# Kernel tuning notes

Hardware: AMD Instinct MI355X
Metric: run time of the kernel (lower is better)

## Reference

```python
import jax, jax.numpy as jnp
import numpy as np

N, L, H, DH = 4, 1024, 16, 64
D = H * DH  # 1024
DFF = 4 * D
NEG_INF = jnp.float32(-1e30)  # used via actual -inf per torch masked_fill


def layer_norm(x, g, b, eps=1e-5):
    mu = jnp.mean(x, axis=-1, keepdims=True)
    var = jnp.mean(jnp.square(x - mu), axis=-1, keepdims=True)
    return (x - mu) * jax.lax.rsqrt(var + eps) * g + b


def mha(q_in, k_in, Wq, Wk, Wv, mask, padding_mask):
    # q_in: (N,Lq,D), k_in: (N,Lk,D); Linear weights (D,D), out = x @ W.T
    n, Lq, _ = q_in.shape
    Lk = k_in.shape[1]
    q = jnp.einsum('nld,od->nlo', q_in, Wq).reshape(n, Lq, H, DH)
    k = jnp.einsum('nld,od->nlo', k_in, Wk).reshape(n, Lk, H, DH)
    v = jnp.einsum('nld,od->nlo', k_in, Wv).reshape(n, Lk, H, DH)
    # per-sample scaling = sqrt(#non-padded keys)
    scaling = jnp.sqrt(jnp.sum(~padding_mask, axis=-1).astype(q.dtype))  # (N,)
    score = jnp.einsum('nqhd,nkhd->nhqk', q, k) / scaling[:, None, None, None]
    if mask is not None:
        score = jnp.where(mask[None, None, :, :], -jnp.inf, score)
    score = jnp.where(padding_mask[:, None, None, :], -jnp.inf, score)
    p = jax.nn.softmax(score, axis=-1)
    out = jnp.einsum('nhqk,nkhd->nqhd', p, v).reshape(n, Lq, D)
    return out


def setup_inputs() -> dict:
    key = jax.random.key(0)
    ks = jax.random.split(key, 16)
    s = 0.02
    inp = {
        'encoded': jax.random.normal(ks[0], (N, L, D), jnp.float32),
        'Y': jax.random.normal(ks[1], (N, L, D), jnp.float32),
        # causal mask: True above diagonal -> attention set to -inf
        'mask': ~jnp.tril(jnp.ones((L, L), dtype=bool)),
        # suffix padding with varied per-sample lengths (all >= 1)
        'padding_mask': jnp.arange(L)[None, :] >= jnp.array([L, 3 * L // 4, L // 2, 7 * L // 8])[:, None],
        # masked self-attention projections
        'Wq1': jax.random.normal(ks[2], (D, D), jnp.float32) * s,
        'Wk1': jax.random.normal(ks[3], (D, D), jnp.float32) * s,
        'Wv1': jax.random.normal(ks[4], (D, D), jnp.float32) * s,
        'g1': jnp.ones((D,), jnp.float32), 'b1': jnp.zeros((D,), jnp.float32),
        # cross-attention projections
        'Wq2': jax.random.normal(ks[5], (D, D), jnp.float32) * s,
        'Wk2': jax.random.normal(ks[6], (D, D), jnp.float32) * s,
        'Wv2': jax.random.normal(ks[7], (D, D), jnp.float32) * s,
        'g2': jnp.ones((D,), jnp.float32), 'b2': jnp.zeros((D,), jnp.float32),
        # FFN
        'We': jax.random.normal(ks[8], (DFF, D), jnp.float32) * s,
        'be': jnp.zeros((DFF,), jnp.float32),
        'Wc': jax.random.normal(ks[9], (D, DFF), jnp.float32) * s,
        'bc': jnp.zeros((D,), jnp.float32),
        'g3': jnp.ones((D,), jnp.float32), 'b3': jnp.zeros((D,), jnp.float32),
    }
    return inp


def reference(encoded, Y, mask, padding_mask,
              Wq1, Wk1, Wv1, g1, b1,
              Wq2, Wk2, Wv2, g2, b2,
              We, be, Wc, bc, g3, b3):
    # masked self-attention + residual + LN (dropout=0 -> identity)
    res = Y
    a = mha(Y, Y, Wq1, Wk1, Wv1, mask, padding_mask)
    Y = layer_norm(a + res, g1, b1)
    # cross-attention (no causal mask) + residual + LN
    res = Y
    a = mha(Y, encoded, Wq2, Wk2, Wv2, None, padding_mask)
    Y = layer_norm(a + res, g2, b2)
    # FFN + residual + LN
    res = Y
    h = jax.nn.relu(jnp.einsum('nld,fd->nlf', Y, We) + be)
    h = jnp.einsum('nlf,df->nld', h, Wc) + bc
    Y = layer_norm(h + res, g3, b3)
    return Y
```

## Files before the change

kernel.cpp:

```cpp
#include <hip/hip_runtime.h>
#include <stdint.h>

#define NB 4
#define LS 1024
#define HH 16
#define DHD 64
#define DM 1024
#define DF 4096
#define QKS 2048
#define LOG2E 1.4426950408889634f

typedef unsigned short u16;
typedef __attribute__((ext_vector_type(4))) float f32x4;
typedef __attribute__((ext_vector_type(8))) __bf16 bf16x8;
typedef __attribute__((ext_vector_type(8))) unsigned short u16x8;

__device__ __forceinline__ u16 f2bf(float f) {
  union { float f; uint32_t u; } v; v.f = f;
  uint32_t u = v.u;
  return (u16)((u + 0x7fffu + ((u >> 16) & 1u)) >> 16);
}

__device__ __forceinline__ bf16x8 ldb8(const u16* p) {
  u16x8 r = *(const u16x8*)p;
  return __builtin_bit_cast(bf16x8, r);
}

__device__ __forceinline__ void gload_lds16(const u16* g, u16* l) {
  __builtin_amdgcn_global_load_lds((const __attribute__((address_space(1))) void*)g,
                                   (__attribute__((address_space(3))) void*)l,
                                   16, 0, 0);
}

#define WAITV8() asm volatile("s_waitcnt vmcnt(8)" ::: "memory")
#define WAITV0() asm volatile("s_waitcnt vmcnt(0)" ::: "memory")
#define WAITLGKM() asm volatile("s_waitcnt lgkmcnt(0)" ::: "memory")
#define PHASE_BARRIER()                        \
  do {                                         \
    WAITLGKM();                                \
    __builtin_amdgcn_sched_barrier(0);         \
    __builtin_amdgcn_s_barrier();              \
    __builtin_amdgcn_sched_barrier(0);         \
  } while (0)

__global__ void prep_kernel(const uint32_t* __restrict__ pm, int* lens, float* iscl) {
  __shared__ int flagByte;
  __shared__ int red[256];
  const int tid = threadIdx.x, n = blockIdx.x;
  if (tid == 0) flagByte = 0;
  __syncthreads();
  int f = 0;
  for (int w = tid; w < (NB * LS) / 4; w += 256) {
    uint32_t u = pm[w];
    if (u != 0u && u != 1u && u != 0x3f800000u) f = 1;
  }
  if (f) atomicOr(&flagByte, 1);
  __syncthreads();
  int c = 0;
  if (flagByte) {
    const uint8_t* pb = (const uint8_t*)pm;
    for (int l = tid; l < LS; l += 256) c += (pb[n * LS + l] == 0) ? 1 : 0;
  } else {
    for (int l = tid; l < LS; l += 256) c += (pm[n * LS + l] == 0) ? 1 : 0;
  }
  red[tid] = c;
  __syncthreads();
  for (int s = 128; s > 0; s >>= 1) {
    if (tid < s) red[tid] += red[tid + s];
    __syncthreads();
  }
  if (tid == 0) { lens[n] = red[0]; iscl[n] = 1.0f / sqrtf((float)red[0]); }
}

__global__ void cvt_all(const float* s0, u16* d0, const float* s1, u16* d1,
                        const float* s2, u16* d2, const float* s3, u16* d3,
                        const float* s4, u16* d4, const float* s5, u16* d5,
                        const float* s6, u16* d6, const float* s7, u16* d7,
                        const float* s8, u16* d8, const float* s9, u16* d9) {
  const int total = 5767168;
  int i = blockIdx.x * 256 + threadIdx.x;
  for (; i < total; i += gridDim.x * 256) {
    const float* s; u16* d; int j;
    if (i < 1048576)      { s = s0; d = d0; j = i; }
    else if (i < 2097152) { s = s1; d = d1; j = i - 1048576; }
    else if (i < 2359296) { s = s2; d = d2; j = i - 2097152; }
    else if (i < 2621440) { s = s3; d = d3; j = i - 2359296; }
    else if (i < 2883584) { s = s4; d = d4; j = i - 2621440; }
    else if (i < 3145728) { s = s5; d = d5; j = i - 2883584; }
    else if (i < 3407872) { s = s6; d = d6; j = i - 3145728; }
    else if (i < 3670016) { s = s7; d = d7; j = i - 3407872; }
    else if (i < 4718592) { s = s8; d = d8; j = i - 3670016; }
    else                  { s = s9; d = d9; j = i - 4718592; }
    float4 fv = ((const float4*)s)[j];
    ushort4 o;
    o.x = f2bf(fv.x); o.y = f2bf(fv.y); o.z = f2bf(fv.z); o.w = f2bf(fv.w);
    ((ushort4*)d)[j] = o;
  }
}

template <int MODE>
__global__ __launch_bounds__(512, 2) void gemm8(
    const u16* __restrict__ P0, const u16* __restrict__ P1,
    const u16* __restrict__ PW, const float* __restrict__ bias,
    void* __restrict__ O0, void* __restrict__ O1,
    void* __restrict__ O2, void* __restrict__ O3,
    const float* __restrict__ iscl) {
  extern __shared__ u16 lds[];
  constexpr int NT = 16;
  const int bm = blockIdx.x;
  const int tid = threadIdx.x;
  const int wid = tid >> 6, lane = tid & 63;
  const int lrow = lane & 15, lgrp = lane >> 4;
  const int wm = wid >> 2, wn = wid & 3;

  const u16* Asrc; const u16* Bsrc; int lda, ldb;
  if constexpr (MODE == 0) {
    Asrc = P0 + (size_t)bm * 256 * DM; lda = DM;
    Bsrc = PW + (size_t)blockIdx.y * 256 * DM; ldb = DM;
  } else if constexpr (MODE == 1) {
    const int z = blockIdx.z;
    Asrc = P0 + (size_t)bm * 256 * DF + z * 1024; lda = DF;
    Bsrc = PW + (size_t)blockIdx.y * 256 * DF + z * 1024; ldb = DF;
  } else {
    const int bnt = blockIdx.y;
    Asrc = (bnt < 12 ? P0 : P1) + (size_t)bm * 256 * DM; lda = DM;
    const int wrow = (bnt < 12) ? bnt * 256 : 4096 + (bnt - 12) * 256;
    Bsrc = PW + (size_t)wrow * DM; ldb = DM;
  }

  int srow[2], skk[2];
#pragma unroll
  for (int i = 0; i < 2; i++) {
    const int c = (i * 8 + wid) * 64 + lane;
    const int pair = c >> 3;
    const int ue = ((c & 7) * 8) ^ ((pair & 7) << 3);
    srow[i] = pair * 2 + (ue >> 5);
    skk[i] = ue & 31;
  }
  const int dslot0 = wid * 512;
  const int dslot1 = (8 + wid) * 512;

  f32x4 acc[2][4][4] = {};

  auto STAGE_A = [&](int kt, int buf, int kh) {
    const int ks = kt < NT ? kt : NT - 1;
    gload_lds16(Asrc + (size_t)srow[0] * lda + ks * 64 + kh * 32 + skk[0],
                lds + buf * 16384 + kh * 8192 + dslot0);
    gload_lds16(Asrc + (size_t)srow[1] * lda + ks * 64 + kh * 32 + skk[1],
                lds + buf * 16384 + kh * 8192 + dslot1);
  };
  auto STAGE_B = [&](int kt, int buf, int kh) {
    const int ks = kt < NT ? kt : NT - 1;
    gload_lds16(Bsrc + (size_t)srow[0] * ldb + ks * 64 + kh * 32 + skk[0],
                lds + 32768 + buf * 16384 + kh * 8192 + dslot0);
    gload_lds16(Bsrc + (size_t)srow[1] * ldb + ks * 64 + kh * 32 + skk[1],
                lds + 32768 + buf * 16384 + kh * 8192 + dslot1);
  };
  auto LDA = [&](int buf, int kh, int mh, bf16x8* a) {
#pragma unroll
    for (int m = 0; m < 4; m++) {
      const int row = wm * 128 + mh * 64 + m * 16 + lrow;
      const int idx = buf * 16384 + kh * 8192 + (row >> 1) * 64 +
                      ((((row & 1) << 5) + (lgrp << 3)) ^ (((row >> 1) & 7) << 3));
      a[m] = ldb8(lds + idx);
    }
  };
  auto LDB = [&](int buf, int kh, bf16x8* b) {
#pragma unroll
    for (int nn = 0; nn < 4; nn++) {
      const int row = wn * 64 + nn * 16 + lrow;
      const int idx = 32768 + buf * 16384 + kh * 8192 + (row >> 1) * 64 +
                      ((((row & 1) << 5) + (lgrp << 3)) ^ (((row >> 1) & 7) << 3));
      b[nn] = ldb8(lds + idx);
    }
  };
  auto MFMA16 = [&](f32x4 (&a4)[4][4], bf16x8* af, bf16x8* bk) {
    __builtin_amdgcn_s_setprio(1);
#pragma unroll
    for (int m = 0; m < 4; m++)
#pragma unroll
      for (int nn = 0; nn < 4; nn++)
        a4[m][nn] = __builtin_amdgcn_mfma_f32_16x16x32_bf16(af[m], bk[nn], a4[m][nn], 0, 0, 0);
    __builtin_amdgcn_s_setprio(0);
  };

  STAGE_A(0, 0, 0); STAGE_B(0, 0, 0);
  STAGE_A(0, 0, 1); STAGE_B(0, 0, 1);
  STAGE_A(1, 1, 0); STAGE_B(1, 1, 0);
  WAITV8();
  __builtin_amdgcn_s_barrier();
  __builtin_amdgcn_sched_barrier(0);

  for (int t = 0; t < NT; t++) {
    const int b = t & 1;
    bf16x8 af[4], bk[4];
    LDA(b, 0, 0, af); LDB(b, 0, bk);
    STAGE_A(t + 1, b ^ 1, 1);
    PHASE_BARRIER();
    MFMA16(acc[0], af, bk);
    LDA(b, 0, 1, af);
    STAGE_B(t + 1, b ^ 1, 1);
    WAITV8();
    PHASE_BARRIER();
    MFMA16(acc[1], af, bk);
    LDA(b, 1, 0, af); LDB(b, 1, bk);
    STAGE_A(t + 2, b, 0);
    PHASE_BARRIER();
    MFMA16(acc[0], af, bk);
    LDA(b, 1, 1, af);
    STAGE_B(t + 2, b, 0);
    WAITV8();
    PHASE_BARRIER();
    MFMA16(acc[1], af, bk);
  }
  WAITV0();

#pragma unroll
  for (int mh = 0; mh < 2; mh++)
#pragma unroll
    for (int m = 0; m < 4; m++) {
      const int grow0 = bm * 256 + wm * 128 + mh * 64 + m * 16 + lgrp * 4;
#pragma unroll
      for (int nn = 0; nn < 4; nn++) {
        const int col_l = wn * 64 + nn * 16 + lrow;
        f32x4 v = acc[mh][m][nn];
        if constexpr (MODE == 0) {
          const int col = blockIdx.y * 256 + col_l;
          const float bv = bias[col];
#pragma unroll
          for (int r = 0; r < 4; r++) {
            float x = v[r] + bv;
            x = x > 0.0f ? x : 0.0f;
            ((u16*)O0)[(size_t)(grow0 + r) * DF + col] = f2bf(x);
          }
        } else if constexpr (MODE == 1) {
          float* C = (float*)O0 + (size_t)blockIdx.z * ((size_t)NB * LS * DM);
          const int col = blockIdx.y * 256 + col_l;
#pragma unroll
          for (int r = 0; r < 4; r++) C[(size_t)(grow0 + r) * DM + col] = v[r];
        } else {
          const int bnt = blockIdx.y;
          const int nidx = grow0 >> 10, l0 = grow0 & 1023;
          if (bnt < 8) {
            const float qs = (bnt < 4) ? iscl[nidx] * LOG2E : 1.0f;
            const int col = bnt * 256 + col_l;
#pragma unroll
            for (int r = 0; r < 4; r++)
              ((u16*)O0)[(size_t)(grow0 + r) * QKS + col] = f2bf(v[r] * qs);
          } else if (bnt < 12) {
            const int vc = (bnt - 8) * 256 + col_l;
            ushort4 o;
            o.x = f2bf(v[0]); o.y = f2bf(v[1]); o.z = f2bf(v[2]); o.w = f2bf(v[3]);
            *(ushort4*)((u16*)O1 + (((size_t)(nidx * HH + (vc >> 6)) * DHD + (vc & 63)) << 10) + l0) = o;
          } else {
            const int col = 1024 + (bnt - 12) * 256 + col_l;
#pragma unroll
            for (int r = 0; r < 4; r++)
              ((u16*)O2)[(size_t)(grow0 + r) * QKS + col] = f2bf(v[r]);
          }
        }
      }
    }
}

__global__ __launch_bounds__(256) void gemm_qv(const u16* __restrict__ Ya,
                                               const u16* __restrict__ Ea,
                                               const u16* __restrict__ Wq,
                                               const u16* __restrict__ Wv,
                                               u16* __restrict__ QKb,
                                               u16* __restrict__ VtB,
                                               const float* __restrict__ iscl) {
  __shared__ u16 Al[128 * 32];
  __shared__ u16 Bl[128 * 32];
  const int tid = threadIdx.x;
  const int bm = blockIdx.x, bnr = blockIdx.y;
  const bool isV = bnr >= 8;
  const int bn = isV ? bnr - 8 : bnr;
  const int wave = tid >> 6, lane = tid & 63;
  const int lrow = lane & 15, lgrp = lane >> 4;
  const int wr = (wave >> 1) * 64, wc = (wave & 1) * 64;
  f32x4 acc[4][4] = {};
  const u16* Ab = (isV ? Ea : Ya) + (size_t)bm * 128 * DM;
  const u16* Bb = (isV ? Wv : Wq) + (size_t)bn * 128 * DM;
  {
    const int c0 = wave, c1 = wave + 4;
    const int r0 = c0 * 16 + (lane >> 2), r1 = c1 * 16 + (lane >> 2);
    const int scc = (lane & 3) * 8;
    const u16* Ag0 = Ab + (size_t)r0 * DM + scc;
    const u16* Ag1 = Ab + (size_t)r1 * DM + scc;
    const u16* Bg0 = Bb + (size_t)r0 * DM + scc;
    const u16* Bg1 = Bb + (size_t)r1 * DM + scc;
    u16* Ad0 = Al + c0 * 512;
    u16* Ad1 = Al + c1 * 512;
    u16* Bd0 = Bl + c0 * 512;
    u16* Bd1 = Bl + c1 * 512;
    for (int kb = 0; kb < DM; kb += 32) {
      gload_lds16(Ag0, Ad0);
      gload_lds16(Ag1, Ad1);
      gload_lds16(Bg0, Bd0);
      gload_lds16(Bg1, Bd1);
      Ag0 += 32; Ag1 += 32; Bg0 += 32; Bg1 += 32;
      __syncthreads();
      bf16x8 af[4], bfr[4];
#pragma unroll
      for (int m = 0; m < 4; m++) af[m] = ldb8(Al + (wr + m * 16 + lrow) * 32 + lgrp * 8);
#pragma unroll
      for (int nn = 0; nn < 4; nn++) bfr[nn] = ldb8(Bl + (wc + nn * 16 + lrow) * 32 + lgrp * 8);
#pragma unroll
      for (int m = 0; m < 4; m++)
#pragma unroll
        for (int nn = 0; nn < 4; nn++)
          acc[m][nn] = __builtin_amdgcn_mfma_f32_16x16x32_bf16(af[m], bfr[nn], acc[m][nn], 0, 0, 0);
      __syncthreads();
    }
  }
#pragma unroll
  for (int m = 0; m < 4; m++) {
    const int row0 = bm * 128 + wr + m * 16 + lgrp * 4;
    const int nidx = row0 >> 10, l0 = row0 & (LS - 1);
#pragma unroll
    for (int nn = 0; nn < 4; nn++) {
      const int col = bn * 128 + wc + nn * 16 + lrow;
      if (!isV) {
        const float qs = iscl[nidx] * LOG2E;
#pragma unroll
        for (int r = 0; r < 4; r++)
          QKb[(size_t)(row0 + r) * QKS + col] = f2bf(acc[m][nn][r] * qs);
      } else {
        const int hh = col >> 6, dd = col & 63;
        ushort4 o;
        o.x = f2bf(acc[m][nn][0]); o.y = f2bf(acc[m][nn][1]);
        o.z = f2bf(acc[m][nn][2]); o.w = f2bf(acc[m][nn][3]);
        *(ushort4*)(VtB + (((size_t)(nidx * HH + hh) * DHD + dd) << 10) + l0) = o;
      }
    }
  }
}

template <bool CAUSAL>
__global__ __launch_bounds__(256) void attn_kernel(const u16* __restrict__ QK,
                                                   const u16* __restrict__ Vt,
                                                   float* __restrict__ Out,
                                                   const int* __restrict__ lens) {
  __shared__ u16 Kl[64 * 72];
  __shared__ u16 Vl[64 * 72];
  __shared__ u16 Pl[4][16 * 72];
  const int n = blockIdx.z, h = blockIdx.y, qb = blockIdx.x * 64;
  const int tid = threadIdx.x, wave = tid >> 6, lane = tid & 63;
  const int lrow = lane & 15, lgrp = lane >> 4;
  const int len = lens[n];
  const int qrow = qb + wave * 16 + lrow;
  const u16* qptr = QK + ((size_t)(n * LS + qrow)) * QKS + h * DHD + lgrp * 8;
  bf16x8 qf0 = ldb8(qptr);
  bf16x8 qf1 = ldb8(qptr + 32);
  f32x4 oacc[4] = {};
  float m_run = -1e30f, l_run = 0.0f;
  const int kend = CAUSAL ? (len < qb + 64 ? len : qb + 64) : len;
  const int srow = tid >> 3, sc = (tid & 7) * 8;
  const u16* kg_base = QK + 1024 + ((size_t)(n * LS)) * QKS + h * DHD + sc;
  const u16* vg_base = Vt + ((size_t)((n * HH + h) * DHD) + srow) * LS + sc;
  u16* pw = Pl[wave];
  u16x8 kreg[2], vreg[2];
  auto LOADKV = [&](int kb) {
#pragma unroll
    for (int i = 0; i < 2; i++) {
      kreg[i] = *(const u16x8*)(kg_base + (size_t)(kb + srow + i * 32) * QKS);
      vreg[i] = *(const u16x8*)(vg_base + (size_t)(i * 32) * LS + kb);
    }
  };
  LOADKV(0);
  for (int kb = 0; kb < kend; kb += 64) {
    __syncthreads();
#pragma unroll
    for (int i = 0; i < 2; i++) {
      *(u16x8*)(Kl + (srow + i * 32) * 72 + sc) = kreg[i];
      *(u16x8*)(Vl + (srow + i * 32) * 72 + sc) = vreg[i];
    }
    __syncthreads();
    if (kb + 64 < kend) LOADKV(kb + 64);
    f32x4 s[4];
#pragma unroll
    for (int st = 0; st < 4; st++) {
      const u16* kr = Kl + (st * 16 + lrow) * 72 + lgrp * 8;
      bf16x8 kf0 = ldb8(kr);
      bf16x8 kf1 = ldb8(kr + 32);
      f32x4 z = {};
      z = __builtin_amdgcn_mfma_f32_16x16x32_bf16(kf0, qf0, z, 0, 0, 0);
      s[st] = __builtin_amdgcn_mfma_f32_16x16x32_bf16(kf1, qf1, z, 0, 0, 0);
    }
    const bool needMask = (kb + 64 > len) || (CAUSAL && (kb + 64 > qb + wave * 16));
    if (needMask) {
#pragma unroll
      for (int st = 0; st < 4; st++)
#pragma unroll
        for (int r = 0; r < 4; r++) {
          const int k = kb + st * 16 + lgrp * 4 + r;
          bool ok = (k < len) && (!CAUSAL || k <= qrow);
          s[st][r] = ok ? s[st][r] : -1e30f;
        }
    }
    float pmax = s[0][0];
#pragma unroll
    for (int st = 0; st < 4; st++)
#pragma unroll
      for (int r = 0; r < 4; r++) pmax = fmaxf(pmax, s[st][r]);
    pmax = fmaxf(pmax, __shfl_xor(pmax, 16));
    pmax = fmaxf(pmax, __shfl_xor(pmax, 32));
    const bool skip = __all(pmax <= m_run + 11.541560327f);
    float fac = 1.0f;
    if (!skip) {
      float mn = fmaxf(m_run, pmax);
      fac = exp2f(m_run - mn);
      m_run = mn;
    }
    float sm = 0.0f;
#pragma unroll
    for (int st = 0; st < 4; st++)
#pragma unroll
      for (int r = 0; r < 4; r++) {
        float p = exp2f(s[st][r] - m_run);
        s[st][r] = p;
        sm += p;
      }
    sm += __shfl_xor(sm, 16);
    sm += __shfl_xor(sm, 32);
    l_run = l_run * fac + sm;
    if (!skip) {
#pragma unroll
      for (int r = 0; r < 4; r++) {
        float fr = __shfl(fac, (lane & 48) | (lgrp * 4 + r));
#pragma unroll
        for (int dt = 0; dt < 4; dt++) oacc[dt][r] *= fr;
      }
    }
#pragma unroll
    for (int st = 0; st < 4; st++) {
      uint32_t w0, w1;
      asm("v_cvt_pk_bf16_f32 %0, %1, %2" : "=v"(w0) : "v"(s[st][0]), "v"(s[st][1]));
      asm("v_cvt_pk_bf16_f32 %0, %1, %2" : "=v"(w1) : "v"(s[st][2]), "v"(s[st][3]));
      uint2 wv; wv.x = w0; wv.y = w1;
      *(uint2*)(pw + lrow * 72 + st * 16 + lgrp * 4) = wv;
    }
#pragma unroll
    for (int ks = 0; ks < 2; ks++) {
      bf16x8 pf = ldb8(pw + lrow * 72 + ks * 32 + lgrp * 8);
#pragma unroll
      for (int dt = 0; dt < 4; dt++) {
        bf16x8 vf = ldb8(Vl + (dt * 16 + lrow) * 72 + ks * 32 + lgrp * 8);
        oacc[dt] = __builtin_amdgcn_mfma_f32_16x16x32_bf16(pf, vf, oacc[dt], 0, 0, 0);
      }
    }
  }
#pragma unroll
  for (int r = 0; r < 4; r++) {
    float lr = __shfl(l_run, (lane & 48) | (lgrp * 4 + r));
    float inv = 1.0f / lr;
    const int row = qb + wave * 16 + lgrp * 4 + r;
    float* op = Out + ((size_t)(n * LS + row)) * DM + h * DHD;
#pragma unroll
    for (int dt = 0; dt < 4; dt++) op[dt * 16 + lrow] = oacc[dt][r] * inv;
  }
}

__global__ __launch_bounds__(256) void ln_kernel(const float* __restrict__ a,
                                                 const float* __restrict__ res,
                                                 const float* __restrict__ g,
                                                 const float* __restrict__ bta,
                                                 float* __restrict__ outf,
                                                 u16* __restrict__ outb) {
  const int row = blockIdx.x, tid = threadIdx.x;
  float4 x = ((const float4*)(a + (size_t)row * DM))[tid];
  float4 rr = ((const float4*)(res + (size_t)row * DM))[tid];
  x.x += rr.x; x.y += rr.y; x.z += rr.z; x.w += rr.w;
  float s = x.x + x.y + x.z + x.w;
  float s2 = x.x * x.x + x.y * x.y + x.z * x.z + x.w * x.w;
#pragma unroll
  for (int m = 1; m < 64; m <<= 1) { s += __shfl_xor(s, m); s2 += __shfl_xor(s2, m); }
  __shared__ float sm[8];
  const int wv = tid >> 6;
  if ((tid & 63) == 0) { sm[wv] = s; sm[4 + wv] = s2; }
  __syncthreads();
  s = sm[0] + sm[1] + sm[2] + sm[3];
  s2 = sm[4] + sm[5] + sm[6] + sm[7];
  const float mean = s * (1.0f / (float)DM);
  const float var = s2 * (1.0f / (float)DM) - mean * mean;
  const float inv = rsqrtf(var + 1e-5f);
  float4 gg = ((const float4*)g)[tid];
  float4 bb = ((const float4*)bta)[tid];
  float4 y;
  y.x = (x.x - mean) * inv * gg.x + bb.x;
  y.y = (x.y - mean) * inv * gg.y + bb.y;
  y.z = (x.z - mean) * inv * gg.z + bb.z;
  y.w = (x.w - mean) * inv * gg.w + bb.w;
  ((float4*)(outf + (size_t)row * DM))[tid] = y;
  if (outb) {
    ushort4 o;
    o.x = f2bf(y.x); o.y = f2bf(y.y); o.z = f2bf(y.z); o.w = f2bf(y.w);
    ((ushort4*)(outb + (size_t)row * DM))[tid] = o;
  }
}

__global__ __launch_bounds__(256) void ln_final(const float* __restrict__ part,
                                                const float* __restrict__ bias,
                                                const float* __restrict__ res,
                                                const float* __restrict__ g,
                                                const float* __restrict__ bta,
                                                float* __restrict__ outf) {
  const int row = blockIdx.x, tid = threadIdx.x;
  const size_t PS = (size_t)NB * LS * DM;
  float4 x = ((const float4*)(part + (size_t)row * DM))[tid];
  float4 p1 = ((const float4*)(part + PS + (size_t)row * DM))[tid];
  float4 p2 = ((const float4*)(part + 2 * PS + (size_t)row * DM))[tid];
  float4 p3 = ((const float4*)(part + 3 * PS + (size_t)row * DM))[tid];
  float4 bb4 = ((const float4*)bias)[tid];
  float4 rr = ((const float4*)(res + (size_t)row * DM))[tid];
  x.x += p1.x + p2.x + p3.x + bb4.x + rr.x;
  x.y += p1.y + p2.y + p3.y + bb4.y + rr.y;
  x.z += p1.z + p2.z + p3.z + bb4.z + rr.z;
  x.w += p1.w + p2.w + p3.w + bb4.w + rr.w;
  float s = x.x + x.y + x.z + x.w;
  float s2 = x.x * x.x + x.y * x.y + x.z * x.z + x.w * x.w;
#pragma unroll
  for (int m = 1; m < 64; m <<= 1) { s += __shfl_xor(s, m); s2 += __shfl_xor(s2, m); }
  __shared__ float sm[8];
  const int wv = tid >> 6;
  if ((tid & 63) == 0) { sm[wv] = s; sm[4 + wv] = s2; }
  __syncthreads();
  s = sm[0] + sm[1] + sm[2] + sm[3];
  s2 = sm[4] + sm[5] + sm[6] + sm[7];
  const float mean = s * (1.0f / (float)DM);
  const float var = s2 * (1.0f / (float)DM) - mean * mean;
  const float inv = rsqrtf(var + 1e-5f);
  float4 gg = ((const float4*)g)[tid];
  float4 bb = ((const float4*)bta)[tid];
  float4 y;
  y.x = (x.x - mean) * inv * gg.x + bb.x;
  y.y = (x.y - mean) * inv * gg.y + bb.y;
  y.z = (x.z - mean) * inv * gg.z + bb.z;
  y.w = (x.w - mean) * inv * gg.w + bb.w;
  ((float4*)(outf + (size_t)row * DM))[tid] = y;
}

extern "C" void kernel_launch(void* const* d_in, const int* in_sizes, int n_in,
                              void* d_out, int out_size, void* d_ws, size_t ws_size,
                              hipStream_t stream) {
  const float* enc = (const float*)d_in[0];
  const float* Yin = (const float*)d_in[1];
  const uint32_t* pmask = (const uint32_t*)d_in[3];
  const float* Wq1 = (const float*)d_in[4];
  const float* Wk1 = (const float*)d_in[5];
  const float* Wv1 = (const float*)d_in[6];
  const float* g1 = (const float*)d_in[7];
  const float* b1 = (const float*)d_in[8];
  const float* Wq2 = (const float*)d_in[9];
  const float* Wk2 = (const float*)d_in[10];
  const float* Wv2 = (const float*)d_in[11];
  const float* g2 = (const float*)d_in[12];
  const float* b2 = (const float*)d_in[13];
  const float* We = (const float*)d_in[14];
  const float* be = (const float*)d_in[15];
  const float* Wc = (const float*)d_in[16];
  const float* bc = (const float*)d_in[17];
  const float* g3 = (const float*)d_in[18];
  const float* b3 = (const float*)d_in[19];

  const size_t ACT = (size_t)NB * LS * DM;
  const size_t WSZ = (size_t)DM * DM;
  const size_t WFF = (size_t)DF * DM;
  const size_t HID = (size_t)NB * LS * DF;

  char* ws = (char*)d_ws;
  size_t off = 0;
  auto alloc = [&](size_t bytes) -> void* {
    void* p = ws + off;
    off += (bytes + 255) & ~(size_t)255;
    return p;
  };
  int* lens = (int*)alloc(64);
  float* iscl = (float*)alloc(64);
  u16* Ybf = (u16*)alloc(ACT * 2);
  u16* Ebf = (u16*)alloc(ACT * 2);
  u16* W6 = (u16*)alloc(WSZ * 6 * 2);
  u16* Web = (u16*)alloc(WFF * 2);
  u16* Wcb = (u16*)alloc(WFF * 2);
  size_t region0 = off;
  u16* QKa = (u16*)alloc((size_t)NB * LS * QKS * 2);
  u16* VtA = (u16*)alloc(ACT * 2);
  u16* QKb = (u16*)alloc((size_t)NB * LS * QKS * 2);
  u16* VtB = (u16*)alloc(ACT * 2);
  float* aout = (float*)alloc(ACT * 4);
  float* y2 = (float*)alloc(ACT * 4);
  float* part = (float*)(ws + region0);
  float* y3 = (float*)alloc(ACT * 4);
  u16* Hb = (u16*)alloc(HID * 2);

  prep_kernel<<<NB, 256, 0, stream>>>(pmask, lens, iscl);
  cvt_all<<<2048, 256, 0, stream>>>(Yin, Ybf, enc, Ebf,
                                    Wq1, W6 + 0 * WSZ, Wk1, W6 + 1 * WSZ,
                                    Wv1, W6 + 2 * WSZ, Wq2, W6 + 3 * WSZ,
                                    Wk2, W6 + 4 * WSZ, Wv2, W6 + 5 * WSZ,
                                    We, Web, Wc, Wcb);

  dim3 blk(256);
  gemm8<2><<<dim3(16, 16), 512, 131072, stream>>>(Ybf, Ebf, W6, nullptr,
                                                  QKa, VtA, QKb, VtB, iscl);
  attn_kernel<true><<<dim3(16, 16, 4), blk, 0, stream>>>(QKa, VtA, aout, lens);
  ln_kernel<<<NB * LS, 256, 0, stream>>>(aout, Yin, g1, b1, y2, Ybf);
  gemm_qv<<<dim3(32, 16), blk, 0, stream>>>(Ybf, Ebf, W6 + 3 * WSZ, W6 + 5 * WSZ,
                                            QKb, VtB, iscl);
  attn_kernel<false><<<dim3(16, 16, 4), blk, 0, stream>>>(QKb, VtB, aout, lens);
  ln_kernel<<<NB * LS, 256, 0, stream>>>(aout, y2, g2, b2, y3, Ebf);
  gemm8<0><<<dim3(16, 16), 512, 131072, stream>>>(Ebf, nullptr, Web, be,
                                                  Hb, nullptr, nullptr, nullptr, nullptr);
  gemm8<1><<<dim3(16, 4, 4), 512, 131072, stream>>>(Hb, nullptr, Wcb, nullptr,
                                                    part, nullptr, nullptr, nullptr, nullptr);
  ln_final<<<NB * LS, 256, 0, stream>>>(part, bc, y3, g3, b3, (float*)d_out);
}
```

Baseline: 287.5 us.

## Widen attention key tile to 128 and store FFN split-K partials in bf16

```diff
diff --git a/kernel.cpp b/kernel.cpp
--- a/kernel.cpp
+++ b/kernel.cpp
@@ -19,6 +19,11 @@
   union { float f; uint32_t u; } v; v.f = f;
   uint32_t u = v.u;
   return (u16)((u + 0x7fffu + ((u >> 16) & 1u)) >> 16);
+}
+
+__device__ __forceinline__ float b2f(u16 u) {
+  union { uint32_t u; float f; } v; v.u = (uint32_t)u << 16;
+  return v.f;
 }
 
 __device__ __forceinline__ bf16x8 ldb8(const u16* p) {
@@ -234,10 +239,10 @@
             ((u16*)O0)[(size_t)(grow0 + r) * DF + col] = f2bf(x);
           }
         } else if constexpr (MODE == 1) {
-          float* C = (float*)O0 + (size_t)blockIdx.z * ((size_t)NB * LS * DM);
+          u16* C = (u16*)O0 + (size_t)blockIdx.z * ((size_t)NB * LS * DM);
           const int col = blockIdx.y * 256 + col_l;
 #pragma unroll
-          for (int r = 0; r < 4; r++) C[(size_t)(grow0 + r) * DM + col] = v[r];
+          for (int r = 0; r < 4; r++) C[(size_t)(grow0 + r) * DM + col] = f2bf(v[r]);
         } else {
           const int bnt = blockIdx.y;
           const int nidx = grow0 >> 10, l0 = grow0 & 1023;
@@ -342,9 +347,9 @@
                                                    const u16* __restrict__ Vt,
                                                    float* __restrict__ Out,
                                                    const int* __restrict__ lens) {
-  __shared__ u16 Kl[64 * 72];
-  __shared__ u16 Vl[64 * 72];
-  __shared__ u16 Pl[4][16 * 72];
+  __shared__ u16 Kl[128 * 72];
+  __shared__ u16 Vl[64 * 136];
+  __shared__ u16 Pl[4][16 * 136];
   const int n = blockIdx.z, h = blockIdx.y, qb = blockIdx.x * 64;
   const int tid = threadIdx.x, wave = tid >> 6, lane = tid & 63;
   const int lrow = lane & 15, lgrp = lane >> 4;
@@ -356,31 +361,32 @@
   f32x4 oacc[4] = {};
   float m_run = -1e30f, l_run = 0.0f;
   const int kend = CAUSAL ? (len < qb + 64 ? len : qb + 64) : len;
-  const int srow = tid >> 3, sc = (tid & 7) * 8;
-  const u16* kg_base = QK + 1024 + ((size_t)(n * LS)) * QKS + h * DHD + sc;
-  const u16* vg_base = Vt + ((size_t)((n * HH + h) * DHD) + srow) * LS + sc;
+  const u16* kg_base = QK + 1024 + ((size_t)(n * LS + (tid >> 3))) * QKS + h * DHD + (tid & 7) * 8;
+  const u16* vg_base = Vt + ((size_t)((n * HH + h) * DHD) + (tid >> 4)) * LS + (tid & 15) * 8;
+  const int klw = (tid >> 3) * 72 + (tid & 7) * 8;
+  const int vlw = (tid >> 4) * 136 + (tid & 15) * 8;
   u16* pw = Pl[wave];
-  u16x8 kreg[2], vreg[2];
+  u16x8 kreg[4], vreg[4];
   auto LOADKV = [&](int kb) {
 #pragma unroll
-    for (int i = 0; i < 2; i++) {
-      kreg[i] = *(const u16x8*)(kg_base + (size_t)(kb + srow + i * 32) * QKS);
-      vreg[i] = *(const u16x8*)(vg_base + (size_t)(i * 32) * LS + kb);
+    for (int i = 0; i < 4; i++) {
+      kreg[i] = *(const u16x8*)(kg_base + (size_t)(kb + i * 32) * QKS);
+      vreg[i] = *(const u16x8*)(vg_base + (size_t)(i * 16) * LS + kb);
     }
   };
   LOADKV(0);
-  for (int kb = 0; kb < kend; kb += 64) {
+  for (int kb = 0; kb < kend; kb += 128) {
     __syncthreads();
 #pragma unroll
-    for (int i = 0; i < 2; i++) {
-      *(u16x8*)(Kl + (srow + i * 32) * 72 + sc) = kreg[i];
-      *(u16x8*)(Vl + (srow + i * 32) * 72 + sc) = vreg[i];
+    for (int i = 0; i < 4; i++) {
+      *(u16x8*)(Kl + klw + i * (32 * 72)) = kreg[i];
+      *(u16x8*)(Vl + vlw + i * (16 * 136)) = vreg[i];
     }
     __syncthreads();
-    if (kb + 64 < kend) LOADKV(kb + 64);
-    f32x4 s[4];
-#pragma unroll
-    for (int st = 0; st < 4; st++) {
+    if (kb + 128 < kend) LOADKV(kb + 128);
+    f32x4 s[8];
+#pragma unroll
+    for (int st = 0; st < 8; st++) {
       const u16* kr = Kl + (st * 16 + lrow) * 72 + lgrp * 8;
       bf16x8 kf0 = ldb8(kr);
       bf16x8 kf1 = ldb8(kr + 32);
@@ -388,10 +394,10 @@
       z = __builtin_amdgcn_mfma_f32_16x16x32_bf16(kf0, qf0, z, 0, 0, 0);
       s[st] = __builtin_amdgcn_mfma_f32_16x16x32_bf16(kf1, qf1, z, 0, 0, 0);
     }
-    const bool needMask = (kb + 64 > len) || (CAUSAL && (kb + 64 > qb + wave * 16));
+    const bool needMask = (kb + 128 > len) || (CAUSAL && (kb + 128 > qb + wave * 16));
     if (needMask) {
 #pragma unroll
-      for (int st = 0; st < 4; st++)
+      for (int st = 0; st < 8; st++)
 #pragma unroll
         for (int r = 0; r < 4; r++) {
           const int k = kb + st * 16 + lgrp * 4 + r;
@@ -401,7 +407,7 @@
     }
     float pmax = s[0][0];
 #pragma unroll
-    for (int st = 0; st < 4; st++)
+    for (int st = 0; st < 8; st++)
 #pragma unroll
       for (int r = 0; r < 4; r++) pmax = fmaxf(pmax, s[st][r]);
     pmax = fmaxf(pmax, __shfl_xor(pmax, 16));
@@ -415,7 +421,7 @@
     }
     float sm = 0.0f;
 #pragma unroll
-    for (int st = 0; st < 4; st++)
+    for (int st = 0; st < 8; st++)
 #pragma unroll
       for (int r = 0; r < 4; r++) {
         float p = exp2f(s[st][r] - m_run);
@@ -434,19 +440,19 @@
       }
     }
 #pragma unroll
-    for (int st = 0; st < 4; st++) {
+    for (int st = 0; st < 8; st++) {
       uint32_t w0, w1;
       asm("v_cvt_pk_bf16_f32 %0, %1, %2" : "=v"(w0) : "v"(s[st][0]), "v"(s[st][1]));
       asm("v_cvt_pk_bf16_f32 %0, %1, %2" : "=v"(w1) : "v"(s[st][2]), "v"(s[st][3]));
       uint2 wv; wv.x = w0; wv.y = w1;
-      *(uint2*)(pw + lrow * 72 + st * 16 + lgrp * 4) = wv;
-    }
-#pragma unroll
-    for (int ks = 0; ks < 2; ks++) {
-      bf16x8 pf = ldb8(pw + lrow * 72 + ks * 32 + lgrp * 8);
+      *(uint2*)(pw + lrow * 136 + st * 16 + lgrp * 4) = wv;
+    }
+#pragma unroll
+    for (int ks = 0; ks < 4; ks++) {
+      bf16x8 pf = ldb8(pw + lrow * 136 + ks * 32 + lgrp * 8);
 #pragma unroll
       for (int dt = 0; dt < 4; dt++) {
-        bf16x8 vf = ldb8(Vl + (dt * 16 + lrow) * 72 + ks * 32 + lgrp * 8);
+        bf16x8 vf = ldb8(Vl + (dt * 16 + lrow) * 136 + ks * 32 + lgrp * 8);
         oacc[dt] = __builtin_amdgcn_mfma_f32_16x16x32_bf16(pf, vf, oacc[dt], 0, 0, 0);
       }
     }
@@ -500,7 +506,7 @@
   }
 }
 
-__global__ __launch_bounds__(256) void ln_final(const float* __restrict__ part,
+__global__ __launch_bounds__(256) void ln_final(const u16* __restrict__ part,
                                                 const float* __restrict__ bias,
                                                 const float* __restrict__ res,
                                                 const float* __restrict__ g,
@@ -508,16 +514,17 @@
                                                 float* __restrict__ outf) {
   const int row = blockIdx.x, tid = threadIdx.x;
   const size_t PS = (size_t)NB * LS * DM;
-  float4 x = ((const float4*)(part + (size_t)row * DM))[tid];
-  float4 p1 = ((const float4*)(part + PS + (size_t)row * DM))[tid];
-  float4 p2 = ((const float4*)(part + 2 * PS + (size_t)row * DM))[tid];
-  float4 p3 = ((const float4*)(part + 3 * PS + (size_t)row * DM))[tid];
+  ushort4 q0 = ((const ushort4*)(part + (size_t)row * DM))[tid];
+  ushort4 q1 = ((const ushort4*)(part + PS + (size_t)row * DM))[tid];
+  ushort4 q2 = ((const ushort4*)(part + 2 * PS + (size_t)row * DM))[tid];
+  ushort4 q3 = ((const ushort4*)(part + 3 * PS + (size_t)row * DM))[tid];
   float4 bb4 = ((const float4*)bias)[tid];
   float4 rr = ((const float4*)(res + (size_t)row * DM))[tid];
-  x.x += p1.x + p2.x + p3.x + bb4.x + rr.x;
-  x.y += p1.y + p2.y + p3.y + bb4.y + rr.y;
-  x.z += p1.z + p2.z + p3.z + bb4.z + rr.z;
-  x.w += p1.w + p2.w + p3.w + bb4.w + rr.w;
+  float4 x;
+  x.x = b2f(q0.x) + b2f(q1.x) + b2f(q2.x) + b2f(q3.x) + bb4.x + rr.x;
+  x.y = b2f(q0.y) + b2f(q1.y) + b2f(q2.y) + b2f(q3.y) + bb4.y + rr.y;
+  x.z = b2f(q0.z) + b2f(q1.z) + b2f(q2.z) + b2f(q3.z) + bb4.z + rr.z;
+  x.w = b2f(q0.w) + b2f(q1.w) + b2f(q2.w) + b2f(q3.w) + bb4.w + rr.w;
   float s = x.x + x.y + x.z + x.w;
   float s2 = x.x * x.x + x.y * x.y + x.z * x.z + x.w * x.w;
 #pragma unroll
@@ -590,7 +597,7 @@
   u16* VtB = (u16*)alloc(ACT * 2);
   float* aout = (float*)alloc(ACT * 4);
   float* y2 = (float*)alloc(ACT * 4);
-  float* part = (float*)(ws + region0);
+  u16* part = (u16*)(ws + region0);
   float* y3 = (float*)alloc(ACT * 4);
   u16* Hb = (u16*)alloc(HID * 2);
 
```

Result: no change. 291.0 us (+1.2%).

## Double attention query rows per wave and store split-K partials in bf16

Applied to the files above, without the earlier changes.

```diff
diff --git a/kernel.cpp b/kernel.cpp
--- a/kernel.cpp
+++ b/kernel.cpp
@@ -19,6 +19,11 @@
   union { float f; uint32_t u; } v; v.f = f;
   uint32_t u = v.u;
   return (u16)((u + 0x7fffu + ((u >> 16) & 1u)) >> 16);
+}
+
+__device__ __forceinline__ float b2f(u16 u) {
+  union { uint32_t u; float f; } v; v.u = (uint32_t)u << 16;
+  return v.f;
 }
 
 __device__ __forceinline__ bf16x8 ldb8(const u16* p) {
@@ -234,10 +239,10 @@
             ((u16*)O0)[(size_t)(grow0 + r) * DF + col] = f2bf(x);
           }
         } else if constexpr (MODE == 1) {
-          float* C = (float*)O0 + (size_t)blockIdx.z * ((size_t)NB * LS * DM);
+          u16* C = (u16*)O0 + (size_t)blockIdx.z * ((size_t)NB * LS * DM);
           const int col = blockIdx.y * 256 + col_l;
 #pragma unroll
-          for (int r = 0; r < 4; r++) C[(size_t)(grow0 + r) * DM + col] = v[r];
+          for (int r = 0; r < 4; r++) C[(size_t)(grow0 + r) * DM + col] = f2bf(v[r]);
         } else {
           const int bnt = blockIdx.y;
           const int nidx = grow0 >> 10, l0 = grow0 & 1023;
@@ -344,18 +349,20 @@
                                                    const int* __restrict__ lens) {
   __shared__ u16 Kl[64 * 72];
   __shared__ u16 Vl[64 * 72];
-  __shared__ u16 Pl[4][16 * 72];
-  const int n = blockIdx.z, h = blockIdx.y, qb = blockIdx.x * 64;
+  __shared__ u16 Pl[4][32 * 72];
+  const int n = blockIdx.z, h = blockIdx.y, qb = blockIdx.x * 128;
   const int tid = threadIdx.x, wave = tid >> 6, lane = tid & 63;
   const int lrow = lane & 15, lgrp = lane >> 4;
   const int len = lens[n];
-  const int qrow = qb + wave * 16 + lrow;
-  const u16* qptr = QK + ((size_t)(n * LS + qrow)) * QKS + h * DHD + lgrp * 8;
-  bf16x8 qf0 = ldb8(qptr);
-  bf16x8 qf1 = ldb8(qptr + 32);
-  f32x4 oacc[4] = {};
-  float m_run = -1e30f, l_run = 0.0f;
-  const int kend = CAUSAL ? (len < qb + 64 ? len : qb + 64) : len;
+  const int q0 = qb + wave * 32;
+  const int qrowA = q0 + lrow, qrowB = qrowA + 16;
+  const u16* qpA = QK + ((size_t)(n * LS + qrowA)) * QKS + h * DHD + lgrp * 8;
+  const u16* qpB = qpA + (size_t)16 * QKS;
+  bf16x8 qA0 = ldb8(qpA), qA1 = ldb8(qpA + 32);
+  bf16x8 qB0 = ldb8(qpB), qB1 = ldb8(qpB + 32);
+  f32x4 oA[4] = {}, oB[4] = {};
+  float mA = -1e30f, lA = 0.0f, mB = -1e30f, lB = 0.0f;
+  const int kend = CAUSAL ? (len < qb + 128 ? len : qb + 128) : len;
   const int srow = tid >> 3, sc = (tid & 7) * 8;
   const u16* kg_base = QK + 1024 + ((size_t)(n * LS)) * QKS + h * DHD + sc;
   const u16* vg_base = Vt + ((size_t)((n * HH + h) * DHD) + srow) * LS + sc;
@@ -378,87 +385,139 @@
     }
     __syncthreads();
     if (kb + 64 < kend) LOADKV(kb + 64);
-    f32x4 s[4];
+    f32x4 sA[4], sB[4];
 #pragma unroll
     for (int st = 0; st < 4; st++) {
       const u16* kr = Kl + (st * 16 + lrow) * 72 + lgrp * 8;
       bf16x8 kf0 = ldb8(kr);
       bf16x8 kf1 = ldb8(kr + 32);
       f32x4 z = {};
-      z = __builtin_amdgcn_mfma_f32_16x16x32_bf16(kf0, qf0, z, 0, 0, 0);
-      s[st] = __builtin_amdgcn_mfma_f32_16x16x32_bf16(kf1, qf1, z, 0, 0, 0);
-    }
-    const bool needMask = (kb + 64 > len) || (CAUSAL && (kb + 64 > qb + wave * 16));
-    if (needMask) {
+      z = __builtin_amdgcn_mfma_f32_16x16x32_bf16(kf0, qA0, z, 0, 0, 0);
+      sA[st] = __builtin_amdgcn_mfma_f32_16x16x32_bf16(kf1, qA1, z, 0, 0, 0);
+      f32x4 y = {};
+      y = __builtin_amdgcn_mfma_f32_16x16x32_bf16(kf0, qB0, y, 0, 0, 0);
+      sB[st] = __builtin_amdgcn_mfma_f32_16x16x32_bf16(kf1, qB1, y, 0, 0, 0);
+    }
+    if ((kb + 64 > len) || (CAUSAL && (kb + 64 > q0))) {
 #pragma unroll
       for (int st = 0; st < 4; st++)
 #pragma unroll
         for (int r = 0; r < 4; r++) {
           const int k = kb + st * 16 + lgrp * 4 + r;
-          bool ok = (k < len) && (!CAUSAL || k <= qrow);
-          s[st][r] = ok ? s[st][r] : -1e30f;
+          if (!((k < len) && (!CAUSAL || k <= qrowA))) sA[st][r] = -1e30f;
+          if (!((k < len) && (!CAUSAL || k <= qrowB))) sB[st][r] = -1e30f;
         }
     }
-    float pmax = s[0][0];
-#pragma unroll
-    for (int st = 0; st < 4; st++)
-#pragma unroll
-      for (int r = 0; r < 4; r++) pmax = fmaxf(pmax, s[st][r]);
-    pmax = fmaxf(pmax, __shfl_xor(pmax, 16));
-    pmax = fmaxf(pmax, __shfl_xor(pmax, 32));
-    const bool skip = __all(pmax <= m_run + 11.541560327f);
-    float fac = 1.0f;
-    if (!skip) {
-      float mn = fmaxf(m_run, pmax);
-      fac = exp2f(m_run - mn);
-      m_run = mn;
-    }
-    float sm = 0.0f;
-#pragma unroll
-    for (int st = 0; st < 4; st++)
-#pragma unroll
-      for (int r = 0; r < 4; r++) {
-        float p = exp2f(s[st][r] - m_run);
-        s[st][r] = p;
-        sm += p;
+    {
+      float pmax = sA[0][0];
+#pragma unroll
+      for (int st = 0; st < 4; st++)
+#pragma unroll
+        for (int r = 0; r < 4; r++) pmax = fmaxf(pmax, sA[st][r]);
+      pmax = fmaxf(pmax, __shfl_xor(pmax, 16));
+      pmax = fmaxf(pmax, __shfl_xor(pmax, 32));
+      const bool skip = __all(pmax <= mA + 11.541560327f);
+      float fac = 1.0f;
+      if (!skip) {
+        float mn = fmaxf(mA, pmax);
+        fac = exp2f(mA - mn);
+        mA = mn;
       }
-    sm += __shfl_xor(sm, 16);
-    sm += __shfl_xor(sm, 32);
-    l_run = l_run * fac + sm;
-    if (!skip) {
-#pragma unroll
-      for (int r = 0; r < 4; r++) {
-        float fr = __shfl(fac, (lane & 48) | (lgrp * 4 + r));
-#pragma unroll
-        for (int dt = 0; dt < 4; dt++) oacc[dt][r] *= fr;
+      float sm = 0.0f;
+#pragma unroll
+      for (int st = 0; st < 4; st++)
+#pragma unroll
+        for (int r = 0; r < 4; r++) {
+          float p = exp2f(sA[st][r] - mA);
+          sA[st][r] = p;
+          sm += p;
+        }
+      sm += __shfl_xor(sm, 16);
+      sm += __shfl_xor(sm, 32);
+      lA = lA * fac + sm;
+      if (!skip) {
+#pragma unroll
+        for (int r = 0; r < 4; r++) {
+          float fr = __shfl(fac, (lane & 48) | (lgrp * 4 + r));
+#pragma unroll
+          for (int dt = 0; dt < 4; dt++) oA[dt][r] *= fr;
+        }
       }
     }
+    {
+      float pmax = sB[0][0];
+#pragma unroll
+      for (int st = 0; st < 4; st++)
+#pragma unroll
+        for (int r = 0; r < 4; r++) pmax = fmaxf(pmax, sB[st][r]);
+      pmax = fmaxf(pmax, __shfl_xor(pmax, 16));
+      pmax = fmaxf(pmax, __shfl_xor(pmax, 32));
+      const bool skip = __all(pmax <= mB + 11.541560327f);
+      float fac = 1.0f;
+      if (!skip) {
+        float mn = fmaxf(mB, pmax);
+        fac = exp2f(mB - mn);
+        mB = mn;
+      }
+      float sm = 0.0f;
+#pragma unroll
+      for (int st = 0; st < 4; st++)
+#pragma unroll
+        for (int r = 0; r < 4; r++) {
+          float p = exp2f(sB[st][r] - mB);
+          sB[st][r] = p;
+          sm += p;
+        }
+      sm += __shfl_xor(sm, 16);
+      sm += __shfl_xor(sm, 32);
+      lB = lB * fac + sm;
+      if (!skip) {
+#pragma unroll
+        for (int r = 0; r < 4; r++) {
+          float fr = __shfl(fac, (lane & 48) | (lgrp * 4 + r));
+#pragma unroll
+          for (int dt = 0; dt < 4; dt++) oB[dt][r] *= fr;
+        }
+      }
+    }
 #pragma unroll
     for (int st = 0; st < 4; st++) {
-      uint32_t w0, w1;
-      asm("v_cvt_pk_bf16_f32 %0, %1, %2" : "=v"(w0) : "v"(s[st][0]), "v"(s[st][1]));
-      asm("v_cvt_pk_bf16_f32 %0, %1, %2" : "=v"(w1) : "v"(s[st][2]), "v"(s[st][3]));
+      uint32_t w0, w1, x0, x1;
+      asm("v_cvt_pk_bf16_f32 %0, %1, %2" : "=v"(w0) : "v"(sA[st][0]), "v"(sA[st][1]));
+      asm("v_cvt_pk_bf16_f32 %0, %1, %2" : "=v"(w1) : "v"(sA[st][2]), "v"(sA[st][3]));
+      asm("v_cvt_pk_bf16_f32 %0, %1, %2" : "=v"(x0) : "v"(sB[st][0]), "v"(sB[st][1]));
+      asm("v_cvt_pk_bf16_f32 %0, %1, %2" : "=v"(x1) : "v"(sB[st][2]), "v"(sB[st][3]));
       uint2 wv; wv.x = w0; wv.y = w1;
+      uint2 xv; xv.x = x0; xv.y = x1;
       *(uint2*)(pw + lrow * 72 + st * 16 + lgrp * 4) = wv;
+      *(uint2*)(pw + (16 + lrow) * 72 + st * 16 + lgrp * 4) = xv;
     }
 #pragma unroll
     for (int ks = 0; ks < 2; ks++) {
-      bf16x8 pf = ldb8(pw + lrow * 72 + ks * 32 + lgrp * 8);
+      bf16x8 pfA = ldb8(pw + lrow * 72 + ks * 32 + lgrp * 8);
+      bf16x8 pfB = ldb8(pw + (16 + lrow) * 72 + ks * 32 + lgrp * 8);
 #pragma unroll
       for (int dt = 0; dt < 4; dt++) {
         bf16x8 vf = ldb8(Vl + (dt * 16 + lrow) * 72 + ks * 32 + lgrp * 8);
-        oacc[dt] = __builtin_amdgcn_mfma_f32_16x16x32_bf16(pf, vf, oacc[dt], 0, 0, 0);
+        oA[dt] = __builtin_amdgcn_mfma_f32_16x16x32_bf16(pfA, vf, oA[dt], 0, 0, 0);
+        oB[dt] = __builtin_amdgcn_mfma_f32_16x16x32_bf16(pfB, vf, oB[dt], 0, 0, 0);
       }
     }
   }
 #pragma unroll
   for (int r = 0; r < 4; r++) {
-    float lr = __shfl(l_run, (lane & 48) | (lgrp * 4 + r));
-    float inv = 1.0f / lr;
-    const int row = qb + wave * 16 + lgrp * 4 + r;
-    float* op = Out + ((size_t)(n * LS + row)) * DM + h * DHD;
-#pragma unroll
-    for (int dt = 0; dt < 4; dt++) op[dt * 16 + lrow] = oacc[dt][r] * inv;
+    float lrA = __shfl(lA, (lane & 48) | (lgrp * 4 + r));
+    float lrB = __shfl(lB, (lane & 48) | (lgrp * 4 + r));
+    float invA = 1.0f / lrA;
+    float invB = 1.0f / lrB;
+    const int rowA = q0 + lgrp * 4 + r;
+    float* opA = Out + ((size_t)(n * LS + rowA)) * DM + h * DHD;
+    float* opB = opA + (size_t)16 * DM;
+#pragma unroll
+    for (int dt = 0; dt < 4; dt++) {
+      opA[dt * 16 + lrow] = oA[dt][r] * invA;
+      opB[dt * 16 + lrow] = oB[dt][r] * invB;
+    }
   }
 }
 
@@ -500,7 +559,7 @@
   }
 }
 
-__global__ __launch_bounds__(256) void ln_final(const float* __restrict__ part,
+__global__ __launch_bounds__(256) void ln_final(const u16* __restrict__ part,
                                                 const float* __restrict__ bias,
                                                 const float* __restrict__ res,
                                                 const float* __restrict__ g,
@@ -508,16 +567,17 @@
                                                 float* __restrict__ outf) {
   const int row = blockIdx.x, tid = threadIdx.x;
   const size_t PS = (size_t)NB * LS * DM;
-  float4 x = ((const float4*)(part + (size_t)row * DM))[tid];
-  float4 p1 = ((const float4*)(part + PS + (size_t)row * DM))[tid];
-  float4 p2 = ((const float4*)(part + 2 * PS + (size_t)row * DM))[tid];
-  float4 p3 = ((const float4*)(part + 3 * PS + (size_t)row * DM))[tid];
+  ushort4 q0 = ((const ushort4*)(part + (size_t)row * DM))[tid];
+  ushort4 q1 = ((const ushort4*)(part + PS + (size_t)row * DM))[tid];
+  ushort4 q2 = ((const ushort4*)(part + 2 * PS + (size_t)row * DM))[tid];
+  ushort4 q3 = ((const ushort4*)(part + 3 * PS + (size_t)row * DM))[tid];
   float4 bb4 = ((const float4*)bias)[tid];
   float4 rr = ((const float4*)(res + (size_t)row * DM))[tid];
-  x.x += p1.x + p2.x + p3.x + bb4.x + rr.x;
-  x.y += p1.y + p2.y + p3.y + bb4.y + rr.y;
-  x.z += p1.z + p2.z + p3.z + bb4.z + rr.z;
-  x.w += p1.w + p2.w + p3.w + bb4.w + rr.w;
+  float4 x;
+  x.x = b2f(q0.x) + b2f(q1.x) + b2f(q2.x) + b2f(q3.x) + bb4.x + rr.x;
+  x.y = b2f(q0.y) + b2f(q1.y) + b2f(q2.y) + b2f(q3.y) + bb4.y + rr.y;
+  x.z = b2f(q0.z) + b2f(q1.z) + b2f(q2.z) + b2f(q3.z) + bb4.z + rr.z;
+  x.w = b2f(q0.w) + b2f(q1.w) + b2f(q2.w) + b2f(q3.w) + bb4.w + rr.w;
   float s = x.x + x.y + x.z + x.w;
   float s2 = x.x * x.x + x.y * x.y + x.z * x.z + x.w * x.w;
 #pragma unroll
@@ -590,7 +650,7 @@
   u16* VtB = (u16*)alloc(ACT * 2);
   float* aout = (float*)alloc(ACT * 4);
   float* y2 = (float*)alloc(ACT * 4);
-  float* part = (float*)(ws + region0);
+  u16* part = (u16*)(ws + region0);
   float* y3 = (float*)alloc(ACT * 4);
   u16* Hb = (u16*)alloc(HID * 2);
 
@@ -604,11 +664,11 @@
   dim3 blk(256);
   gemm8<2><<<dim3(16, 16), 512, 131072, stream>>>(Ybf, Ebf, W6, nullptr,
                                                   QKa, VtA, QKb, VtB, iscl);
-  attn_kernel<true><<<dim3(16, 16, 4), blk, 0, stream>>>(QKa, VtA, aout, lens);
+  attn_kernel<true><<<dim3(8, 16, 4), blk, 0, stream>>>(QKa, VtA, aout, lens);
   ln_kernel<<<NB * LS, 256, 0, stream>>>(aout, Yin, g1, b1, y2, Ybf);
   gemm_qv<<<dim3(32, 16), blk, 0, stream>>>(Ybf, Ebf, W6 + 3 * WSZ, W6 + 5 * WSZ,
                                             QKb, VtB, iscl);
-  attn_kernel<false><<<dim3(16, 16, 4), blk, 0, stream>>>(QKb, VtB, aout, lens);
+  attn_kernel<false><<<dim3(8, 16, 4), blk, 0, stream>>>(QKb, VtB, aout, lens);
   ln_kernel<<<NB * LS, 256, 0, stream>>>(aout, y2, g2, b2, y3, Ebf);
   gemm8<0><<<dim3(16, 16), 512, 131072, stream>>>(Ebf, nullptr, Web, be,
                                                   Hb, nullptr, nullptr, nullptr, nullptr);
```

Result: no change. 286.0 us (-0.5%).
